# Kernel tuning notes

Hardware: AMD Instinct MI355X
Metric: run time of the kernel (lower is better)

Reference implementation:

```python
import jax, jax.numpy as jnp
import numpy as np

V = 50257; CTX = 2048; D = 1024; H = 16; L = 8; DH = D // H
B = 2; S = 2048; EPS = 1e-5


def setup_inputs() -> dict:
    key = jax.random.key(0)
    ks = jax.random.split(key, 8)
    s = 0.02
    def n(k, shape):
        return jax.random.normal(k, shape, jnp.float32) * s
    return {
        "x": jax.random.randint(ks[0], (B, S), 0, V),
        "wte": n(ks[1], (V, D)),
        "wpe": n(ks[2], (CTX, D)),
        "ln1_g": jnp.ones((L, D), jnp.float32), "ln1_b": jnp.zeros((L, D), jnp.float32),
        "w_qkv": n(ks[3], (L, D, 3 * D)), "b_qkv": jnp.zeros((L, 3 * D), jnp.float32),
        "w_proj": n(ks[4], (L, D, D)), "b_proj": jnp.zeros((L, D), jnp.float32),
        "ln2_g": jnp.ones((L, D), jnp.float32), "ln2_b": jnp.zeros((L, D), jnp.float32),
        "w_fc": n(ks[5], (L, D, 4 * D)), "b_fc": jnp.zeros((L, 4 * D), jnp.float32),
        "w_cp": n(ks[6], (L, 4 * D, D)), "b_cp": jnp.zeros((L, D), jnp.float32),
        "lnf_g": jnp.ones((D,), jnp.float32), "lnf_b": jnp.zeros((D,), jnp.float32),
        "w_head": n(ks[7], (D, V)),
    }


def layernorm(x, g, b):
    m = x.mean(-1, keepdims=True)
    v = ((x - m) ** 2).mean(-1, keepdims=True)
    return (x - m) * jax.lax.rsqrt(v + EPS) * g + b


def gpt_forward(x, wte, wpe, ln1_g, ln1_b, w_qkv, b_qkv, w_proj, b_proj,
                ln2_g, ln2_b, w_fc, b_fc, w_cp, b_cp, lnf_g, lnf_b, w_head):
    Bx, Sx = x.shape
    h = wte[x] + wpe[:Sx]                       # [B,S,D]
    mask = jnp.tril(jnp.ones((Sx, Sx), bool))   # causal mask
    scale = DH ** -0.5

    def block(h, p):
        g1, b1, wq, bq, wp, bp, g2, b2, wf, bf, wc, bc = p
        y = layernorm(h, g1, b1)
        qkv = y @ wq + bq                        # [B,S,3D]
        q, k, v = jnp.split(qkv, 3, axis=-1)
        q = q.reshape(Bx, Sx, H, DH)
        k = k.reshape(Bx, Sx, H, DH)
        v = v.reshape(Bx, Sx, H, DH)
        att = jnp.einsum('bqhd,bkhd->bhqk', q, k) * scale
        att = jnp.where(mask, att, -jnp.inf)
        att = jax.nn.softmax(att, axis=-1)
        z = jnp.einsum('bhqk,bkhd->bqhd', att, v).reshape(Bx, Sx, D)
        h = h + z @ wp + bp
        y2 = layernorm(h, g2, b2)
        h = h + jax.nn.gelu(y2 @ wf + bf, approximate=False) @ wc + bc
        return h, None

    h, _ = jax.lax.scan(block, h, (ln1_g, ln1_b, w_qkv, b_qkv, w_proj, b_proj,
                                   ln2_g, ln2_b, w_fc, b_fc, w_cp, b_cp))
    h = layernorm(h, lnf_g, lnf_b)
    logits = h[:, -1:, :] @ w_head              # [B,1,V] (last position only)
    return logits


def reference(x, wte, wpe, ln1_g, ln1_b, w_qkv, b_qkv, w_proj, b_proj,
              ln2_g, ln2_b, w_fc, b_fc, w_cp, b_cp, lnf_g, lnf_b, w_head):
    return gpt_forward(x, wte, wpe, ln1_g, ln1_b, w_qkv, b_qkv, w_proj, b_proj,
                       ln2_g, ln2_b, w_fc, b_fc, w_cp, b_cp, lnf_g, lnf_b, w_head)
```

## Files before the change

### kernel.cpp

```cpp
#include <hip/hip_runtime.h>
#include <hip/hip_bf16.h>
#include <math.h>

#define VOCAB 50257
#define CTX 2048
#define DMODEL 1024
#define NHEAD 16
#define NLAYER 8
#define DHEAD 64
#define BATCH 2
#define SEQ 2048
#define NTOK (BATCH * SEQ)

typedef __bf16 bf16x8 __attribute__((ext_vector_type(8)));
typedef float  f32x4  __attribute__((ext_vector_type(4)));
typedef unsigned short ushort4v __attribute__((ext_vector_type(4)));
typedef unsigned short ushort8v __attribute__((ext_vector_type(8)));

__device__ inline void gl_lds16(const void* g, void* l) {
    __builtin_amdgcn_global_load_lds(
        (const __attribute__((address_space(1))) unsigned int*)g,
        (__attribute__((address_space(3))) unsigned int*)l, 16, 0, 0);
}

__device__ inline unsigned short f2bs(float v) {
    __hip_bfloat16 t = __float2bfloat16(v);
    return *(unsigned short*)&t;
}

__device__ void embed_body(int t, const int* __restrict__ x,
                           const float* __restrict__ wte,
                           const float* __restrict__ wpe,
                           float* __restrict__ h) {
    int s = t & (SEQ - 1);
    int tok = x[t];
    const float* pe = wpe + (long)s * DMODEL;
    const float* te = wte + (long)tok * DMODEL;
    float* ph = h + (long)t * DMODEL;
    for (int d = threadIdx.x; d < DMODEL; d += 256)
        ph[d] = te[d] + pe[d];
}

__device__ inline float wave_sum(float v) {
    for (int off = 32; off; off >>= 1) v += __shfl_xor(v, off);
    return v;
}

__global__ void ln_std(const float* __restrict__ in, unsigned short* __restrict__ out,
                       const float* __restrict__ g, const float* __restrict__ b) {
    __shared__ float red[4], red2[4];
    int row = blockIdx.x;
    const float* px = in + (long)row * DMODEL;
    unsigned short* po = out + (long)row * DMODEL;
    int tid = threadIdx.x;
    int wid = tid >> 6, lane = tid & 63;

    float x[4];
    float s = 0.f;
    #pragma unroll
    for (int i = 0; i < 4; ++i) { x[i] = px[tid + i * 256]; s += x[i]; }
    s = wave_sum(s);
    if (lane == 0) red[wid] = s;
    __syncthreads();
    float mean = (red[0] + red[1] + red[2] + red[3]) * (1.0f / DMODEL);

    float s2 = 0.f;
    #pragma unroll
    for (int i = 0; i < 4; ++i) { float d = x[i] - mean; s2 += d * d; }
    s2 = wave_sum(s2);
    if (lane == 0) red2[wid] = s2;
    __syncthreads();
    float var = (red2[0] + red2[1] + red2[2] + red2[3]) * (1.0f / DMODEL);
    float r = 1.0f / sqrtf(var + 1e-5f);
    #pragma unroll
    for (int i = 0; i < 4; ++i) {
        int d = tid + i * 256;
        po[d] = f2bs((x[i] - mean) * r * g[d] + b[d]);
    }
}

__global__ void ln_final(const float* __restrict__ in, float* __restrict__ out,
                         const float* __restrict__ g, const float* __restrict__ b,
                         long row_stride) {
    __shared__ float red[4], red2[4];
    int row = blockIdx.x;
    const float* px = in + (long)row * row_stride;
    float* po = out + (long)row * DMODEL;
    int tid = threadIdx.x;
    int wid = tid >> 6, lane = tid & 63;
    float x[4];
    float s = 0.f;
    #pragma unroll
    for (int i = 0; i < 4; ++i) { x[i] = px[tid + i * 256]; s += x[i]; }
    s = wave_sum(s);
    if (lane == 0) red[wid] = s;
    __syncthreads();
    float mean = (red[0] + red[1] + red[2] + red[3]) * (1.0f / DMODEL);
    float s2 = 0.f;
    #pragma unroll
    for (int i = 0; i < 4; ++i) { float d = x[i] - mean; s2 += d * d; }
    s2 = wave_sum(s2);
    if (lane == 0) red2[wid] = s2;
    __syncthreads();
    float var = (red2[0] + red2[1] + red2[2] + red2[3]) * (1.0f / DMODEL);
    float r = 1.0f / sqrtf(var + 1e-5f);
    #pragma unroll
    for (int i = 0; i < 4; ++i) {
        int d = tid + i * 256;
        po[d] = (x[i] - mean) * r * g[d] + b[d];
    }
}

__device__ void convT_body(char* smem, int kx, int ny, const float* __restrict__ W,
                           unsigned short* __restrict__ WT, int K, int N) {
    float (*t)[65] = (float(*)[65])smem;
    const int k0 = kx * 64, n0 = ny * 64;
    const int tid = threadIdx.x;
    {
        const int krow = tid >> 4, c4 = (tid & 15) * 4;
        #pragma unroll
        for (int p = 0; p < 4; ++p) {
            f32x4 gv = *(const f32x4*)&W[(long)(k0 + p * 16 + krow) * N + n0 + c4];
            #pragma unroll
            for (int j = 0; j < 4; ++j) t[p * 16 + krow][c4 + j] = gv[j];
        }
    }
    __syncthreads();
    {
        const int n = tid >> 3, kl = (tid & 7) * 8;
        #pragma unroll
        for (int p = 0; p < 2; ++p) {
            ushort8v pk;
            #pragma unroll
            for (int j = 0; j < 8; ++j) pk[j] = f2bs(t[kl + j][p * 32 + n]);
            *(ushort8v*)&WT[(long)(n0 + p * 32 + n) * K + k0 + kl] = pk;
        }
    }
}

#define STG_A(KS, H) do { \
    const unsigned short* g_ = A + (long)(bm + (H) * 128 + srow) * K + (KS) * 64 + stgch; \
    unsigned short* s_ = LDS + (((KS) & 1) * 2 + (H)) * 8192 + (w * 8) * 64; \
    gl_lds16(g_, s_); gl_lds16(g_ + 64L * K, s_ + 4096); \
} while (0)
#define STG_B(KS, H) do { \
    const unsigned short* g_ = BT + (long)(bn + (H) * 128 + srow) * K + (KS) * 64 + stgch; \
    unsigned short* s_ = LDS + 32768 + (((KS) & 1) * 2 + (H)) * 8192 + (w * 8) * 64; \
    gl_lds16(g_, s_); gl_lds16(g_ + 64L * K, s_ + 4096); \
} while (0)
#define MM2(M_, x0, x1) do { \
    acc[M_][0] = __builtin_amdgcn_mfma_f32_16x16x32_bf16(x0, bfr[0], acc[M_][0], 0, 0, 0); \
    acc[M_][0] = __builtin_amdgcn_mfma_f32_16x16x32_bf16(x1, bfr[1], acc[M_][0], 0, 0, 0); \
    acc[M_][1] = __builtin_amdgcn_mfma_f32_16x16x32_bf16(x0, bfr[2], acc[M_][1], 0, 0, 0); \
    acc[M_][1] = __builtin_amdgcn_mfma_f32_16x16x32_bf16(x1, bfr[3], acc[M_][1], 0, 0, 0); \
    acc[M_][2] = __builtin_amdgcn_mfma_f32_16x16x32_bf16(x0, bfr[4], acc[M_][2], 0, 0, 0); \
    acc[M_][2] = __builtin_amdgcn_mfma_f32_16x16x32_bf16(x1, bfr[5], acc[M_][2], 0, 0, 0); \
    acc[M_][3] = __builtin_amdgcn_mfma_f32_16x16x32_bf16(x0, bfr[6], acc[M_][3], 0, 0, 0); \
    acc[M_][3] = __builtin_amdgcn_mfma_f32_16x16x32_bf16(x1, bfr[7], acc[M_][3], 0, 0, 0); \
} while (0)
#define PHASE(Q, SPAR, STAGE_STMT, TAIL_STMT) do { \
    bf16x8 a00, a01, a10, a11; \
    if (((Q) & 3) == 0) { \
        const unsigned short* Bb_ = lBp[SPAR] + ((wc & 1) * 64 + fr) * 64; \
        bfr[0] = *(const bf16x8*)(Bb_ + rd0);        bfr[1] = *(const bf16x8*)(Bb_ + rd1); \
        bfr[2] = *(const bf16x8*)(Bb_ + 1024 + rd0); bfr[3] = *(const bf16x8*)(Bb_ + 1024 + rd1); \
        bfr[4] = *(const bf16x8*)(Bb_ + 2048 + rd0); bfr[5] = *(const bf16x8*)(Bb_ + 2048 + rd1); \
        bfr[6] = *(const bf16x8*)(Bb_ + 3072 + rd0); bfr[7] = *(const bf16x8*)(Bb_ + 3072 + rd1); \
    } \
    { const unsigned short* Ab_ = lAp[SPAR] + fr * 64; \
      a00 = *(const bf16x8*)(Ab_ + (((Q) & 3) * 2) * 1024 + rd0); \
      a01 = *(const bf16x8*)(Ab_ + (((Q) & 3) * 2) * 1024 + rd1); \
      a10 = *(const bf16x8*)(Ab_ + (((Q) & 3) * 2 + 1) * 1024 + rd0); \
      a11 = *(const bf16x8*)(Ab_ + (((Q) & 3) * 2 + 1) * 1024 + rd1); } \
    STAGE_STMT; \
    __builtin_amdgcn_s_barrier(); \
    asm volatile("s_waitcnt lgkmcnt(0)" ::: "memory"); \
    __builtin_amdgcn_sched_barrier(0); \
    __builtin_amdgcn_s_setprio(1); \
    MM2(((Q) & 3) * 2, a00, a01); \
    MM2(((Q) & 3) * 2 + 1, a10, a11); \
    __builtin_amdgcn_s_setprio(0); \
    TAIL_STMT; \
    __builtin_amdgcn_s_barrier(); \
} while (0)

template<int EPI>
__global__ __launch_bounds__(512, 1)
void mm_mfma256(const unsigned short* __restrict__ A,
                const unsigned short* __restrict__ BT,
                const float* __restrict__ bias,
                void* __restrict__ Cout, int M, int N, int K, int nbx) {
    extern __shared__ unsigned short LDS[];
    const int tid = threadIdx.x;
    const int w = tid >> 6, lane = tid & 63;
    const int wr = w >> 2, wc = w & 3;
    const int nwg = gridDim.x, bid = blockIdx.x;
    const int swz = (bid & 7) * (nwg >> 3) + (bid >> 3);
    const int bm = (swz / nbx) * 256, bn = (swz % nbx) * 256;

    f32x4 acc[8][4];
    #pragma unroll
    for (int m = 0; m < 8; ++m)
        #pragma unroll
        for (int n = 0; n < 4; ++n)
            acc[m][n] = (f32x4){0.f, 0.f, 0.f, 0.f};

    const int fr = lane & 15, kg = lane >> 4;
    const int rd0 = 8 * (kg ^ (lane & 7)), rd1 = 8 * ((kg + 4) ^ (lane & 7));
    const int stgch = 8 * ((lane & 7) ^ (lane >> 3));
    const int srow = w * 8 + (lane >> 3);
    unsigned short* const lAp[2] = { LDS + wr * 8192, LDS + (2 + wr) * 8192 };
    unsigned short* const lBp[2] = { LDS + 32768 + (wc >> 1) * 8192,
                                     LDS + 32768 + (2 + (wc >> 1)) * 8192 };
    bf16x8 bfr[8];

    STG_B(0, 0); STG_B(0, 1); STG_A(0, 0); STG_A(0, 1); STG_B(1, 0); STG_B(1, 1);
    asm volatile("s_waitcnt vmcnt(4)" ::: "memory");
    __builtin_amdgcn_sched_barrier(0);
    __builtin_amdgcn_s_barrier();

    const int T = K >> 7;
    for (int t = 0; t < T; ++t) {
        const int s = 2 * t;
        const bool nl = (t < T - 1);
        PHASE(0, 0, STG_A(s + 1, 0), );
        PHASE(1, 0, STG_A(s + 1, 1), );
        PHASE(2, 0, if (nl) STG_B(s + 2, 0), );
        PHASE(3, 0, if (nl) STG_B(s + 2, 1),
              if (nl) { asm volatile("s_waitcnt vmcnt(4)" ::: "memory"); } else { asm volatile("s_waitcnt vmcnt(0)" ::: "memory"); } __builtin_amdgcn_sched_barrier(0); );
        PHASE(4, 1, if (nl) STG_A(s + 2, 0), );
        PHASE(5, 1, if (nl) STG_A(s + 2, 1), );
        PHASE(6, 1, if (nl) STG_B(s + 3, 0), );
        PHASE(7, 1, if (nl) STG_B(s + 3, 1),
              if (nl) { asm volatile("s_waitcnt vmcnt(4)" ::: "memory"); __builtin_amdgcn_sched_barrier(0); } );
    }

    const int r0 = (lane >> 4) * 4;
    #pragma unroll
    for (int n = 0; n < 4; ++n) {
        int colb = bn + wc * 64 + n * 16;
        float bv = bias[colb + fr];
        #pragma unroll
        for (int m = 0; m < 8; ++m) {
            int rowb = bm + wr * 128 + m * 16 + r0;
            if (EPI == 3) {
                unsigned short* qkvB = (unsigned short*)Cout;
                int which = colb >> 10, hh = (colb & 1023) >> 6, dbase = colb & 63;
                int b_ = rowb >> 11, s_ = rowb & 2047;
                long bh2 = b_ * 16 + hh;
                float v[4];
                #pragma unroll
                for (int r = 0; r < 4; ++r) v[r] = acc[m][n][r] + bv;
                if (which == 2) {
                    ushort4v pk;
                    #pragma unroll
                    for (int r = 0; r < 4; ++r) pk[r] = f2bs(v[r]);
                    *(ushort4v*)&qkvB[8388608L + (bh2 * 64 + dbase + fr) * 2048 + s_] = pk;
                } else {
                    unsigned short* dst = qkvB + (long)which * 4194304L +
                                          (bh2 * 2048 + s_) * 64 + dbase + fr;
                    #pragma unroll
                    for (int r = 0; r < 4; ++r) dst[r * 64] = f2bs(v[r]);
                }
            } else {
                #pragma unroll
                for (int r = 0; r < 4; ++r) {
                    long row = rowb + r, col = colb + fr;
                    float v = acc[m][n][r] + bv;
                    v = 0.5f * v * (1.0f + erff(v * 0.70710678118f));
                    ((__hip_bfloat16*)Cout)[row * N + col] = __float2bfloat16(v);
                }
            }
        }
    }
}

__device__ void n64_body(char* smem, int bx, int by,
                         const unsigned short* __restrict__ A,
                         const unsigned short* __restrict__ BT,
                         const float* __restrict__ bias, const float* __restrict__ R,
                         float* __restrict__ Cout, int M, int N, int K) {
    unsigned short* As = (unsigned short*)smem;
    unsigned short* Bs = As + 2 * 128 * 32;
    const int tid = threadIdx.x;
    const int w = tid >> 6, lane = tid & 63;
    const int bm = by * 128, bn = bx * 64;
    const int wr = (w >> 1) * 64, wc = (w & 1) * 32;

    f32x4 acc[4][2];
    #pragma unroll
    for (int m = 0; m < 4; ++m)
        #pragma unroll
        for (int n = 0; n < 2; ++n)
            acc[m][n] = (f32x4){0.f, 0.f, 0.f, 0.f};

    const int lrow = lane >> 2;
    const int lcol = (lane & 3) * 8;
    const unsigned short* gA = A + (long)(bm + w * 32 + lrow) * K + lcol;
    const unsigned short* gB = BT + (long)(bn + w * 16 + lrow) * K + lcol;

#define N64_STAGE(K0, BB) do { \
    gl_lds16(gA + (K0),          &As[(BB) * 4096 + (w * 32) * 32]); \
    gl_lds16(gA + (K0) + 16 * K, &As[(BB) * 4096 + (w * 32 + 16) * 32]); \
    gl_lds16(gB + (K0),          &Bs[(BB) * 2048 + (w * 16) * 32]); \
} while (0)

    N64_STAGE(0, 0);
    asm volatile("s_waitcnt vmcnt(0)" ::: "memory");
    __builtin_amdgcn_sched_barrier(0);
    __builtin_amdgcn_s_barrier();

    const int T = K >> 5;
    for (int t = 0; t < T; ++t) {
        const int buf = t & 1;
        if (t + 1 < T) N64_STAGE((t + 1) * 32, buf ^ 1);

        bf16x8 a[4], b[2];
        #pragma unroll
        for (int m = 0; m < 4; ++m)
            a[m] = *(const bf16x8*)&As[buf * 4096 + (wr + m * 16 + (lane & 15)) * 32 + (lane >> 4) * 8];
        #pragma unroll
        for (int n = 0; n < 2; ++n)
            b[n] = *(const bf16x8*)&Bs[buf * 2048 + (wc + n * 16 + (lane & 15)) * 32 + (lane >> 4) * 8];
        #pragma unroll
        for (int m = 0; m < 4; ++m)
            #pragma unroll
            for (int n = 0; n < 2; ++n)
                acc[m][n] = __builtin_amdgcn_mfma_f32_16x16x32_bf16(a[m], b[n], acc[m][n], 0, 0, 0);

        asm volatile("s_waitcnt vmcnt(0)" ::: "memory");
        __builtin_amdgcn_sched_barrier(0);
        __builtin_amdgcn_s_barrier();
    }
#undef N64_STAGE

    const int r0 = (lane >> 4) * 4, cc = lane & 15;
    #pragma unroll
    for (int n = 0; n < 2; ++n) {
        int colb = bn + wc + n * 16;
        float bv = bias[colb + cc];
        #pragma unroll
        for (int m = 0; m < 4; ++m) {
            int rowb = bm + wr + m * 16 + r0;
            #pragma unroll
            for (int r = 0; r < 4; ++r) {
                long row = rowb + r, col = colb + cc;
                float v = acc[m][n][r] + bv + R[row * N + col];
                Cout[row * N + col] = v;
            }
        }
    }
}

__device__ void attn_body(char* smem, int bh, int qb,
                          const unsigned short* __restrict__ qB,
                          const unsigned short* __restrict__ kB,
                          const unsigned short* __restrict__ vT,
                          __hip_bfloat16* __restrict__ z) {
    const int tid = threadIdx.x, w = tid >> 6, lane = tid & 63;
    const int arow = lane & 15, kg = lane >> 4;
    unsigned short* Ks = (unsigned short*)smem;
    unsigned short* Vs = Ks + 128 * 64;
    unsigned short* Ps = Vs + 64 * 128 + w * 16 * 128;

    const long kvbase = (long)bh * (2048 * 64);

    bf16x8 qa[2];
    {
        const unsigned short* q0 = qB + kvbase + (long)(qb + w * 16 + arow) * 64 + kg * 8;
        qa[0] = *(const bf16x8*)(q0);
        qa[1] = *(const bf16x8*)(q0 + 32);
    }

    f32x4 po[4];
    float mrow[4], lrow[4];
    #pragma unroll
    for (int i = 0; i < 4; ++i) {
        po[i] = (f32x4){0.f, 0.f, 0.f, 0.f};
        mrow[i] = -1e30f; lrow[i] = 0.f;
    }

    const int ksrow = lane >> 3;
    const int kschunk = (lane & 7) ^ ksrow;
    const int vsr = lane >> 4;
    const int cmax = qb >> 7;

    for (int c = 0; c <= cmax; ++c) {
        {
            const unsigned short* ks0 = kB + kvbase +
                (long)(c * 128 + w * 32 + ksrow) * 64 + kschunk * 8;
            #pragma unroll
            for (int i = 0; i < 4; ++i)
                gl_lds16(ks0 + (long)i * 8 * 64, &Ks[(w * 32 + i * 8) * 64]);
            #pragma unroll
            for (int i = 0; i < 4; ++i) {
                int d = w * 16 + i * 4 + vsr;
                int sch = (lane & 15) ^ (d & 7);
                gl_lds16(vT + kvbase + (long)d * 2048 + c * 128 + sch * 8,
                         &Vs[(w * 16 + i * 4) * 128]);
            }
        }
        __syncthreads();

        f32x4 s[8];
        #pragma unroll
        for (int n = 0; n < 8; ++n) {
            s[n] = (f32x4){0.f, 0.f, 0.f, 0.f};
            int row = n * 16 + arow, sw = row & 7;
            bf16x8 kb0 = *(const bf16x8*)&Ks[row * 64 + (kg ^ sw) * 8];
            bf16x8 kb1 = *(const bf16x8*)&Ks[row * 64 + ((4 + kg) ^ sw) * 8];
            s[n] = __builtin_amdgcn_mfma_f32_16x16x32_bf16(qa[0], kb0, s[n], 0, 0, 0);
            s[n] = __builtin_amdgcn_mfma_f32_16x16x32_bf16(qa[1], kb1, s[n], 0, 0, 0);
        }

        const bool diag = (c == cmax);
        #pragma unroll
        for (int n = 0; n < 8; ++n)
            #pragma unroll
            for (int r = 0; r < 4; ++r) {
                float v = s[n][r] * 0.125f;
                if (diag) {
                    int key = c * 128 + n * 16 + arow;
                    int qrow = qb + w * 16 + kg * 4 + r;
                    if (key > qrow) v = -1e30f;
                }
                s[n][r] = v;
            }

        #pragma unroll
        for (int r = 0; r < 4; ++r) {
            float rm = s[0][r];
            #pragma unroll
            for (int n = 1; n < 8; ++n) rm = fmaxf(rm, s[n][r]);
            #pragma unroll
            for (int off = 1; off < 16; off <<= 1)
                rm = fmaxf(rm, __shfl_xor(rm, off));
            float mnew = fmaxf(mrow[r], rm);
            float esc = expf(mrow[r] - mnew);
            float rs = 0.f;
            #pragma unroll
            for (int n = 0; n < 8; ++n) {
                float p = expf(s[n][r] - mnew);
                s[n][r] = p;
                rs += p;
            }
            #pragma unroll
            for (int off = 1; off < 16; off <<= 1)
                rs += __shfl_xor(rs, off);
            lrow[r] = lrow[r] * esc + rs;
            #pragma unroll
            for (int dt = 0; dt < 4; ++dt) po[dt][r] *= esc;
            mrow[r] = mnew;
        }

        #pragma unroll
        for (int n = 0; n < 8; ++n) {
            int col = n * 16 + arow;
            int chunk = col >> 3, cw = col & 7;
            #pragma unroll
            for (int r = 0; r < 4; ++r) {
                int row = kg * 4 + r;
                Ps[row * 128 + ((chunk ^ (row & 7)) * 8 + cw)] = f2bs(s[n][r]);
            }
        }

        bf16x8 pa[4];
        #pragma unroll
        for (int ks = 0; ks < 4; ++ks)
            pa[ks] = *(const bf16x8*)&Ps[arow * 128 + (((ks * 4 + kg) ^ (arow & 7)) * 8)];
        #pragma unroll
        for (int dt = 0; dt < 4; ++dt) {
            int vrow = dt * 16 + arow, sw = vrow & 7;
            #pragma unroll
            for (int ks = 0; ks < 4; ++ks) {
                bf16x8 vb = *(const bf16x8*)&Vs[vrow * 128 + (((ks * 4 + kg) ^ sw) * 8)];
                po[dt] = __builtin_amdgcn_mfma_f32_16x16x32_bf16(pa[ks], vb, po[dt], 0, 0, 0);
            }
        }
        __syncthreads();
    }

    const int b_ = bh >> 4, hofs = (bh & 15) * 64;
    #pragma unroll
    for (int dt = 0; dt < 4; ++dt)
        #pragma unroll
        for (int r = 0; r < 4; ++r) {
            long row = (long)b_ * 2048 + qb + w * 16 + kg * 4 + r;
            z[row * 1024 + hofs + dt * 16 + arow] = __float2bfloat16(po[dt][r] / lrow[r]);
        }
}

__global__ __launch_bounds__(256)
void fused_embed_convT(const int* __restrict__ x, const float* __restrict__ wte,
                       const float* __restrict__ wpe, float* __restrict__ h,
                       const float* __restrict__ W, unsigned short* __restrict__ WT,
                       int K, int N, int nEmb) {
    extern __shared__ char smem[];
    int bid = blockIdx.x;
    if (bid < nEmb) {
        embed_body(bid, x, wte, wpe, h);
    } else {
        int r = bid - nEmb, kt = K >> 6;
        convT_body(smem, r % kt, r / kt, W, WT, K, N);
    }
}

__global__ __launch_bounds__(256)
void fused_attn_convT2(const unsigned short* __restrict__ qB,
                       const unsigned short* __restrict__ kB,
                       const unsigned short* __restrict__ vT,
                       __hip_bfloat16* __restrict__ z,
                       const float* __restrict__ W1, unsigned short* __restrict__ WT1,
                       int K1, int N1, int n1,
                       const float* __restrict__ W2, unsigned short* __restrict__ WT2,
                       int K2, int N2, int nAttn) {
    extern __shared__ char smem[];
    int bid = blockIdx.x;
    if (bid < nAttn) {
        attn_body(smem, bid & 31, (bid >> 5) * 64, qB, kB, vT, z);
    } else if (bid < nAttn + n1) {
        int r = bid - nAttn, kt = K1 >> 6;
        convT_body(smem, r % kt, r / kt, W1, WT1, K1, N1);
    } else {
        int r = bid - nAttn - n1, kt = K2 >> 6;
        convT_body(smem, r % kt, r / kt, W2, WT2, K2, N2);
    }
}

__global__ __launch_bounds__(256)
void fused_n64_convT(const unsigned short* __restrict__ A,
                     const unsigned short* __restrict__ BT,
                     const float* __restrict__ bias, const float* __restrict__ R,
                     float* __restrict__ Cout, int M, int N, int K, int nbx,
                     const float* __restrict__ W2, unsigned short* __restrict__ WT2,
                     int K2, int N2, int nMM) {
    extern __shared__ char smem[];
    int bid = blockIdx.x;
    if (bid < nMM) {
        n64_body(smem, bid % nbx, bid / nbx, A, BT, bias, R, Cout, M, N, K);
    } else {
        int r = bid - nMM, kt = K2 >> 6;
        convT_body(smem, r % kt, r / kt, W2, WT2, K2, N2);
    }
}

__global__ void head_kernel(const float* __restrict__ hl, const float* __restrict__ W,
                            float* __restrict__ out) {
    __shared__ float hs[2 * DMODEL];
    int tid = threadIdx.x;
    #pragma unroll
    for (int i = 0; i < 8; ++i) hs[tid + i * 256] = hl[tid + i * 256];
    __syncthreads();
    int v = blockIdx.x * 256 + tid;
    if (v >= VOCAB) return;
    float a0 = 0.f, a1 = 0.f;
    for (int d = 0; d < DMODEL; ++d) {
        float wv = W[(long)d * VOCAB + v];
        a0 += hs[d] * wv;
        a1 += hs[DMODEL + d] * wv;
    }
    out[v] = a0;
    out[VOCAB + v] = a1;
}

extern "C" void kernel_launch(void* const* d_in, const int* in_sizes, int n_in,
                              void* d_out, int out_size, void* d_ws, size_t ws_size,
                              hipStream_t stream) {
    const int*   x      = (const int*)  d_in[0];
    const float* wte    = (const float*)d_in[1];
    const float* wpe    = (const float*)d_in[2];
    const float* ln1_g  = (const float*)d_in[3];
    const float* ln1_b  = (const float*)d_in[4];
    const float* w_qkv  = (const float*)d_in[5];
    const float* b_qkv  = (const float*)d_in[6];
    const float* w_proj = (const float*)d_in[7];
    const float* b_proj = (const float*)d_in[8];
    const float* ln2_g  = (const float*)d_in[9];
    const float* ln2_b  = (const float*)d_in[10];
    const float* w_fc   = (const float*)d_in[11];
    const float* b_fc   = (const float*)d_in[12];
    const float* w_cp   = (const float*)d_in[13];
    const float* b_cp   = (const float*)d_in[14];
    const float* lnf_g  = (const float*)d_in[15];
    const float* lnf_b  = (const float*)d_in[16];
    const float* w_head = (const float*)d_in[17];
    float* out = (float*)d_out;

    char* ws = (char*)d_ws;
    float*          h     = (float*)ws;
    unsigned short* qkvB  = (unsigned short*)(ws + (16L << 20));
    unsigned short* y_bf  = (unsigned short*)(ws + (40L << 20));
    __hip_bfloat16* z_bf  = (__hip_bfloat16*)(ws + (48L << 20));
    unsigned short* fc_bf = (unsigned short*)(ws + (56L << 20));
    unsigned short* wT_a  = (unsigned short*)(ws + (88L << 20));
    unsigned short* wT_b  = (unsigned short*)(ws + (97L << 20));
    unsigned short* wT_c  = (unsigned short*)(ws + (106L << 20));
    unsigned short* wT_q  = (unsigned short*)(ws + (115L << 20));
    float*          hl    = (float*)(ws + (124L << 20));

    const int SM_CONV = 16640;
    const int SM_ATTN = 49152;
    const int SM_N64  = 24576;

    fused_embed_convT<<<4096 + 768, 256, SM_CONV, stream>>>(
        x, wte, wpe, h, w_qkv, wT_q, 1024, 3072, 4096);

    for (int l = 0; l < NLAYER; ++l) {
        ln_std<<<NTOK, 256, 0, stream>>>(h, y_bf, ln1_g + l * DMODEL, ln1_b + l * DMODEL);

        mm_mfma256<3><<<192, 512, 131072, stream>>>(
            y_bf, wT_q, b_qkv + l * 3072, qkvB, NTOK, 3072, 1024, 12);

        fused_attn_convT2<<<1024 + 256 + 1024, 256, SM_ATTN, stream>>>(
            qkvB, qkvB + 4194304L, qkvB + 8388608L, z_bf,
            w_proj + (long)l * DMODEL * DMODEL, wT_b, 1024, 1024, 256,
            w_cp + (long)l * 4096 * DMODEL, wT_c, 4096, 1024, 1024);

        fused_n64_convT<<<512 + 1024, 256, SM_N64, stream>>>(
            (const unsigned short*)z_bf, wT_b, b_proj + l * DMODEL, h, h,
            NTOK, 1024, 1024, 16,
            w_fc + (long)l * DMODEL * 4096, wT_a, 1024, 4096, 512);

        ln_std<<<NTOK, 256, 0, stream>>>(h, y_bf, ln2_g + l * DMODEL, ln2_b + l * DMODEL);

        mm_mfma256<2><<<256, 512, 131072, stream>>>(
            y_bf, wT_a, b_fc + l * 4096, fc_bf, NTOK, 4096, 1024, 16);

        int nConv = (l + 1 < NLAYER) ? 768 : 0;
        fused_n64_convT<<<512 + nConv, 256, SM_N64, stream>>>(
            fc_bf, wT_c, b_cp + l * DMODEL, h, h, NTOK, 1024, 4096, 16,
            w_qkv + (long)(l + 1) * DMODEL * 3072, wT_q, 1024, 3072, 512);
    }

    ln_final<<<BATCH, 256, 0, stream>>>(h + (long)(SEQ - 1) * DMODEL, hl,
                                        lnf_g, lnf_b, (long)SEQ * DMODEL);
    head_kernel<<<(VOCAB + 255) / 256, 256, 0, stream>>>(hl, w_head, out);
}
```

Before: 2.426 ms.

## Widen attention blocks to 128 queries with 512 threads and schedule longest first

The fused attention and weight-transpose kernel now runs 512-thread blocks. Each attention block covers 128 query rows with 8 waves, so every staged K/V chunk is shared by twice as many queries. This halves the number of attention blocks and the K/V global-to-LDS traffic. Query blocks are issued in reverse order so the long causal blocks start first, and the transpose work gets a 512-thread variant. The costs are a larger shared-memory footprint per block (64 KB), possibly lower occupancy, and less parallelism for short-causal tiles.

Result: faster. 2.358 ms (-2.8%).

```diff
diff --git a/kernel.cpp b/kernel.cpp
--- a/kernel.cpp
+++ b/kernel.cpp
@@ -135,6 +135,30 @@
             for (int j = 0; j < 8; ++j) pk[j] = f2bs(t[kl + j][p * 32 + n]);
             *(ushort8v*)&WT[(long)(n0 + p * 32 + n) * K + k0 + kl] = pk;
         }
+    }
+}
+
+__device__ void convT_body512(char* smem, int kx, int ny, const float* __restrict__ W,
+                              unsigned short* __restrict__ WT, int K, int N) {
+    float (*t)[65] = (float(*)[65])smem;
+    const int k0 = kx * 64, n0 = ny * 64;
+    const int tid = threadIdx.x;
+    {
+        const int krow = tid >> 4, c4 = (tid & 15) * 4;
+        #pragma unroll
+        for (int p = 0; p < 2; ++p) {
+            f32x4 gv = *(const f32x4*)&W[(long)(k0 + p * 32 + krow) * N + n0 + c4];
+            #pragma unroll
+            for (int j = 0; j < 4; ++j) t[p * 32 + krow][c4 + j] = gv[j];
+        }
+    }
+    __syncthreads();
+    {
+        const int n = tid >> 3, kl = (tid & 7) * 8;
+        ushort8v pk;
+        #pragma unroll
+        for (int j = 0; j < 8; ++j) pk[j] = f2bs(t[kl + j][n]);
+        *(ushort8v*)&WT[(long)(n0 + n) * K + k0 + kl] = pk;
     }
 }
 
@@ -388,16 +412,16 @@
     for (int c = 0; c <= cmax; ++c) {
         {
             const unsigned short* ks0 = kB + kvbase +
-                (long)(c * 128 + w * 32 + ksrow) * 64 + kschunk * 8;
-            #pragma unroll
-            for (int i = 0; i < 4; ++i)
-                gl_lds16(ks0 + (long)i * 8 * 64, &Ks[(w * 32 + i * 8) * 64]);
-            #pragma unroll
-            for (int i = 0; i < 4; ++i) {
-                int d = w * 16 + i * 4 + vsr;
+                (long)(c * 128 + w * 16 + ksrow) * 64 + kschunk * 8;
+            #pragma unroll
+            for (int i = 0; i < 2; ++i)
+                gl_lds16(ks0 + (long)i * 8 * 64, &Ks[(w * 16 + i * 8) * 64]);
+            #pragma unroll
+            for (int i = 0; i < 2; ++i) {
+                int d = w * 8 + i * 4 + vsr;
                 int sch = (lane & 15) ^ (d & 7);
                 gl_lds16(vT + kvbase + (long)d * 2048 + c * 128 + sch * 8,
-                         &Vs[(w * 16 + i * 4) * 128]);
+                         &Vs[(w * 8 + i * 4) * 128]);
             }
         }
         __syncthreads();
@@ -505,7 +529,7 @@
     }
 }
 
-__global__ __launch_bounds__(256)
+__global__ __launch_bounds__(512)
 void fused_attn_convT2(const unsigned short* __restrict__ qB,
                        const unsigned short* __restrict__ kB,
                        const unsigned short* __restrict__ vT,
@@ -517,13 +541,15 @@
     extern __shared__ char smem[];
     int bid = blockIdx.x;
     if (bid < nAttn) {
-        attn_body(smem, bid & 31, (bid >> 5) * 64, qB, kB, vT, z);
+        int bh = bid & 31;
+        int qblk = 15 - (bid >> 5);
+        attn_body(smem, bh, qblk * 128, qB, kB, vT, z);
     } else if (bid < nAttn + n1) {
         int r = bid - nAttn, kt = K1 >> 6;
-        convT_body(smem, r % kt, r / kt, W1, WT1, K1, N1);
+        convT_body512(smem, r % kt, r / kt, W1, WT1, K1, N1);
     } else {
         int r = bid - nAttn - n1, kt = K2 >> 6;
-        convT_body(smem, r % kt, r / kt, W2, WT2, K2, N2);
+        convT_body512(smem, r % kt, r / kt, W2, WT2, K2, N2);
     }
 }
 
@@ -599,7 +625,7 @@
     float*          hl    = (float*)(ws + (124L << 20));
 
     const int SM_CONV = 16640;
-    const int SM_ATTN = 49152;
+    const int SM_ATTN = 65536;
     const int SM_N64  = 24576;
 
     fused_embed_convT<<<4096 + 768, 256, SM_CONV, stream>>>(
@@ -611,10 +637,10 @@
         mm_mfma256<3><<<192, 512, 131072, stream>>>(
             y_bf, wT_q, b_qkv + l * 3072, qkvB, NTOK, 3072, 1024, 12);
 
-        fused_attn_convT2<<<1024 + 256 + 1024, 256, SM_ATTN, stream>>>(
+        fused_attn_convT2<<<512 + 256 + 1024, 512, SM_ATTN, stream>>>(
             qkvB, qkvB + 4194304L, qkvB + 8388608L, z_bf,
             w_proj + (long)l * DMODEL * DMODEL, wT_b, 1024, 1024, 256,
-            w_cp + (long)l * 4096 * DMODEL, wT_c, 4096, 1024, 1024);
+            w_cp + (long)l * 4096 * DMODEL, wT_c, 4096, 1024, 512);
 
         fused_n64_convT<<<512 + 1024, 256, SM_N64, stream>>>(
             (const unsigned short*)z_bf, wT_b, b_proj + l * DMODEL, h, h,
```
